# Performance work log

Measured on AMD Instinct MI355X. Metric: run time of the kernel, lower is better.

## Reference

```python
import jax, jax.numpy as jnp
import numpy as np

N = 100000
DEG = 16            # edges per source node (1 self-loop + 15 random)
E = N * DEG
IN_F = 128
OUT_F = 64
ALPHA = 0.2         # leaky relu negative slope


def _build_edges(key):
    # edges sorted by src (as adj.nonzero() would be), every node has >=1 out-edge
    src = jnp.repeat(jnp.arange(N, dtype=jnp.int32), DEG)
    dst = jax.random.randint(key, (E,), 0, N, dtype=jnp.int32)
    # force a self-loop as the first edge of every block
    self_pos = jnp.arange(E, dtype=jnp.int32) % DEG == 0
    dst = jnp.where(self_pos, src, dst)
    return jnp.stack([src, dst])  # [2, E]


def setup_inputs() -> dict:
    key = jax.random.key(0)
    k1, k2, k3, k4, k5, k6 = jax.random.split(key, 6)
    return {
        "input": jax.random.normal(k1, (N, IN_F), dtype=jnp.float32),
        "edge": _build_edges(k2),
        "W_high": jax.random.normal(k3, (IN_F, OUT_F), dtype=jnp.float32) * 0.1,
        "W_low": jax.random.normal(k4, (IN_F, OUT_F), dtype=jnp.float32) * 0.1,
        "a_high": jax.random.normal(k5, (1, 2 * OUT_F), dtype=jnp.float32) * 0.1,
        "a_low": jax.random.normal(k6, (1, 2 * OUT_F), dtype=jnp.float32) * 0.1,
    }


def _relu6(x):
    return jnp.clip(x, 0.0, 6.0)


def reference(input, edge, W_high, W_low, a_high, a_low):
    n = input.shape[0]
    src, dst = edge[0], edge[1]

    h_high = input @ W_high          # [N, F]
    h_low = input @ W_low            # [N, F]

    # a.mm(cat(h[src], h[dst]).T) == (h @ a_src)[src] + (h @ a_dst)[dst]
    f = W_high.shape[1]
    s_high = (h_high @ a_high[0, :f])[src] + (h_high @ a_high[0, f:])[dst]  # [E]
    s_low = (h_low @ a_low[0, :f])[src] + (h_low @ a_low[0, f:])[dst]

    edge_e_high = jnp.exp(-jax.nn.leaky_relu(s_high, ALPHA))  # [E], > 0
    edge_e_low = jnp.exp(-jax.nn.leaky_relu(s_low, ALPHA))

    seg = lambda v: jax.ops.segment_sum(v, src, num_segments=n, indices_are_sorted=True)

    # rowsum uses RAW exp values (before relu6/dropout), matching the source
    e_high_rowsum = seg(edge_e_high)[:, None]  # [N, 1]
    e_low_rowsum = seg(edge_e_low)[:, None]

    # relu6 clamp (dropout p=0 -> identity, eval mode)
    eh = _relu6(edge_e_high)
    el = _relu6(edge_e_low)

    # m @ (h[src] +/- h[dst]) == segment_sum over src of per-edge features
    h_agg_high = seg(h_high[src] + h_high[dst])   # [N, F]
    h_agg_low = seg(h_low[src] - h_low[dst])      # [N, F]

    # spmm: out[i] = sum_{(i,j)} e_ij * h_agg[j]
    h_prime_high = seg(eh[:, None] * h_agg_high[dst]) / e_high_rowsum
    h_prime_low = seg(el[:, None] * h_agg_low[dst]) / e_low_rowsum

    h_prime = 0.5 * (h_prime_high + h_prime_low)
    return _relu6(h_prime)  # concat=True
```

## Files before the change

kernel.cpp:

```cpp
#include <hip/hip_runtime.h>

#define N_NODES 100000
#define DEG 16
#define IN_F 128
#define OUT_F 64
#define E_EDGES (N_NODES * DEG)

typedef __bf16 bf16x8 __attribute__((ext_vector_type(8)));
typedef unsigned short u16x8 __attribute__((ext_vector_type(8)));
typedef float f32x4 __attribute__((ext_vector_type(4)));
typedef unsigned int u32x4 __attribute__((ext_vector_type(4)));

union BF8 { u16x8 u; bf16x8 b; };

__device__ inline float lo_bf(unsigned int u) {
    union { unsigned int i; float f; } v; v.i = u << 16; return v.f;
}
__device__ inline float hi_bf(unsigned int u) {
    union { unsigned int i; float f; } v; v.i = u & 0xFFFF0000u; return v.f;
}
__device__ inline unsigned short f2bf(float f) {
    union { float f; unsigned int i; } v; v.f = f;
    return (unsigned short)((v.i + 0x7FFFu + ((v.i >> 16) & 1u)) >> 16);
}
__device__ inline unsigned int packbf(float a, float b) {
    return (unsigned int)f2bf(a) | ((unsigned int)f2bf(b) << 16);
}

__global__ __launch_bounds__(256) void k_wprep(
    const float* __restrict__ Wh, const float* __restrict__ Wl,
    unsigned short* __restrict__ Wimg)
{
    int idx = blockIdx.x * 256 + threadIdx.x;
    int m = idx >> 13;
    int rem = idx & 8191;
    int k = rem >> 6, n = rem & 63;
    float v = m ? Wl[rem] : Wh[rem];
    Wimg[m * 8704 + n * 136 + k] = f2bf(v);
}

__global__ __launch_bounds__(256) void k_gemm(
    const float* __restrict__ in, const unsigned short* __restrict__ Wimg,
    unsigned int* __restrict__ H)
{
    __shared__ __align__(16) unsigned short ldsW[2][64][136];
    __shared__ __align__(16) unsigned short ldsA[64][136];

    {
        const u32x4* src = (const u32x4*)Wimg;
        u32x4* dst = (u32x4*)ldsW;
        for (int i = threadIdx.x; i < 2176; i += 256) dst[i] = src[i];
    }

    int row0B = blockIdx.x * 64;
    {
        const f32x4* src = (const f32x4*)(in + (size_t)row0B * IN_F);
        #pragma unroll
        for (int i = 0; i < 8; i++) {
            int c = threadIdx.x + 256 * i;
            int row = c >> 5;
            int kc = (c & 31) * 4;
            int grow = row0B + row;
            f32x4 v = (grow < N_NODES) ? src[c]
                      : *(const f32x4*)(in + (size_t)(N_NODES - 1) * IN_F + kc);
            unsigned int p0 = packbf(v[0], v[1]);
            unsigned int p1 = packbf(v[2], v[3]);
            *(unsigned int*)&ldsA[row][kc]     = p0;
            *(unsigned int*)&ldsA[row][kc + 2] = p1;
        }
    }
    __syncthreads();

    int wv = threadIdx.x >> 6;
    int lane = threadIdx.x & 63;
    int quad = lane >> 4, c = lane & 15;
    int row0 = row0B + wv * 16;

    bf16x8 afrag[4];
    #pragma unroll
    for (int kb = 0; kb < 4; kb++) {
        BF8 a;
        a.u = *(const u16x8*)&ldsA[wv * 16 + c][kb * 32 + quad * 8];
        afrag[kb] = a.b;
    }

    f32x4 acc[2][4];
    #pragma unroll
    for (int m = 0; m < 2; m++)
        #pragma unroll
        for (int t = 0; t < 4; t++) acc[m][t] = (f32x4){0, 0, 0, 0};

    #pragma unroll
    for (int kb = 0; kb < 4; kb++) {
        #pragma unroll
        for (int t = 0; t < 4; t++) {
            int n = t * 16 + c;
            BF8 bh, bl;
            bh.u = *(const u16x8*)&ldsW[0][n][kb * 32 + quad * 8];
            bl.u = *(const u16x8*)&ldsW[1][n][kb * 32 + quad * 8];
            acc[0][t] = __builtin_amdgcn_mfma_f32_16x16x32_bf16(afrag[kb], bh.b, acc[0][t], 0, 0, 0);
            acc[1][t] = __builtin_amdgcn_mfma_f32_16x16x32_bf16(afrag[kb], bl.b, acc[1][t], 0, 0, 0);
        }
    }

    #pragma unroll
    for (int r = 0; r < 4; r++) {
        int row = row0 + quad * 4 + r;
        if (row >= N_NODES) continue;
        size_t base = (size_t)row * OUT_F + c;
        #pragma unroll
        for (int t = 0; t < 4; t++)
            H[base + t * 16] = packbf(acc[0][t][r], acc[1][t][r]);
    }
}

__global__ __launch_bounds__(256) void k_agg(
    const unsigned int* __restrict__ H, const int* __restrict__ dst,
    const float* __restrict__ ah, const float* __restrict__ al,
    unsigned int* __restrict__ HAGG, f32x4* __restrict__ s)
{
    int lane = threadIdx.x & 63;
    int node = __builtin_amdgcn_readfirstlane(blockIdx.x * 4 + (threadIdx.x >> 6));
    const int* dp = dst + node * DEG;

    unsigned int hu = H[(size_t)node * 64 + lane];
    float hh = lo_bf(hu);
    float hl = hi_bf(hu);
    float sh = 16.0f * hh;
    float sl = 16.0f * hl;

    #pragma unroll
    for (int half = 0; half < 2; half++) {
        unsigned int u[8];
        #pragma unroll
        for (int t = 0; t < 8; t++) {
            int j = dp[half * 8 + t];
            u[t] = H[(size_t)j * 64 + lane];
        }
        #pragma unroll
        for (int t = 0; t < 8; t++) { sh += lo_bf(u[t]); sl -= hi_bf(u[t]); }
    }
    HAGG[(size_t)node * 64 + lane] = packbf(sh, sl);

    float ph = hh * ah[lane];
    float qh = hh * ah[64 + lane];
    float pl = hl * al[lane];
    float ql = hl * al[64 + lane];
    #pragma unroll
    for (int o = 32; o > 0; o >>= 1) {
        ph += __shfl_xor(ph, o);
        qh += __shfl_xor(qh, o);
        pl += __shfl_xor(pl, o);
        ql += __shfl_xor(ql, o);
    }
    if (lane == 0) s[node] = (f32x4){ph, qh, pl, ql};
}

__global__ __launch_bounds__(256) void k_out(
    const unsigned int* __restrict__ HAGG, const int* __restrict__ dst,
    const f32x4* __restrict__ s, float* __restrict__ out)
{
    int lane = threadIdx.x & 63;
    int node = __builtin_amdgcn_readfirstlane(blockIdx.x * 4 + (threadIdx.x >> 6));
    const int* dp = dst + node * DEG;

    int jl = dp[lane & 15];
    f32x4 si = s[node];
    f32x4 sj = s[jl];
    float xh = si.x + sj.y;
    float xl = si.z + sj.w;
    float lh = xh > 0.0f ? xh : 0.2f * xh;
    float ll = xl > 0.0f ? xl : 0.2f * xl;
    float wh = __expf(-lh);
    float wl = __expf(-ll);
    float rh = wh, rl = wl;
    #pragma unroll
    for (int o = 8; o > 0; o >>= 1) { rh += __shfl_xor(rh, o); rl += __shfl_xor(rl, o); }
    float eh = fminf(wh, 6.0f);
    float el = fminf(wl, 6.0f);

    float acc_h = 0.0f, acc_l = 0.0f;
    #pragma unroll
    for (int half = 0; half < 2; half++) {
        unsigned int u[8];
        float weh[8], wel[8];
        #pragma unroll
        for (int t = 0; t < 8; t++) {
            int j = dp[half * 8 + t];
            u[t] = HAGG[(size_t)j * 64 + lane];
        }
        #pragma unroll
        for (int t = 0; t < 8; t++) {
            weh[t] = __shfl(eh, half * 8 + t);
            wel[t] = __shfl(el, half * 8 + t);
        }
        #pragma unroll
        for (int t = 0; t < 8; t++) {
            acc_h += weh[t] * lo_bf(u[t]);
            acc_l += wel[t] * hi_bf(u[t]);
        }
    }
    float r = 0.5f * (acc_h / rh + acc_l / rl);
    r = fminf(fmaxf(r, 0.0f), 6.0f);
    out[(size_t)node * 64 + lane] = r;
}

extern "C" void kernel_launch(void* const* d_in, const int* in_sizes, int n_in,
                              void* d_out, int out_size, void* d_ws, size_t ws_size,
                              hipStream_t stream) {
    const float* input = (const float*)d_in[0];
    const int*   edge  = (const int*)d_in[1];
    const float* Wh    = (const float*)d_in[2];
    const float* Wl    = (const float*)d_in[3];
    const float* ah    = (const float*)d_in[4];
    const float* al    = (const float*)d_in[5];
    float* out = (float*)d_out;

    unsigned int* H    = (unsigned int*)d_ws;
    unsigned int* HAGG = H + (size_t)N_NODES * 64;
    f32x4* s = (f32x4*)(HAGG + (size_t)N_NODES * 64);
    unsigned short* Wimg = (unsigned short*)(s + N_NODES);

    const int* dstp = edge + E_EDGES;

    k_wprep<<<64, 256, 0, stream>>>(Wh, Wl, Wimg);
    k_gemm<<<1563, 256, 0, stream>>>(input, Wimg, H);
    k_agg<<<N_NODES / 4, 256, 0, stream>>>(H, dstp, ah, al, HAGG, s);
    k_out<<<N_NODES / 4, 256, 0, stream>>>(HAGG, dstp, s, out);
}
```

Before: 228.8 us.

## Store aggregated features in feature-group-major layout and split output gather by groups

HAGG is now written in 8 feature-group slabs (each slab holds 8 features per node, 32 bytes), and the output kernel is restructured so each block handles one feature group for 32 nodes, with 8 lanes per node. Keeping each pass over a single group slab shrinks the working set of the random neighbor gathers (1/8 of HAGG per group) so it can stay resident in cache across blocks. The trade-offs are that edge weights (exp/leaky-relu and s lookups) are recomputed 8 times per node, and each gather touches only 32 contiguous bytes per neighbor instead of 256.

```diff
diff --git a/kernel.cpp b/kernel.cpp
--- a/kernel.cpp
+++ b/kernel.cpp
@@ -117,7 +117,7 @@
 __global__ __launch_bounds__(256) void k_agg(
     const unsigned int* __restrict__ H, const int* __restrict__ dst,
     const float* __restrict__ ah, const float* __restrict__ al,
-    unsigned int* __restrict__ HAGG, f32x4* __restrict__ s)
+    unsigned int* __restrict__ HAGG_G, f32x4* __restrict__ s)
 {
     int lane = threadIdx.x & 63;
     int node = __builtin_amdgcn_readfirstlane(blockIdx.x * 4 + (threadIdx.x >> 6));
@@ -140,7 +140,7 @@
         #pragma unroll
         for (int t = 0; t < 8; t++) { sh += lo_bf(u[t]); sl -= hi_bf(u[t]); }
     }
-    HAGG[(size_t)node * 64 + lane] = packbf(sh, sl);
+    HAGG_G[((size_t)(lane >> 3) * N_NODES + node) * 8 + (lane & 7)] = packbf(sh, sl);
 
     float ph = hh * ah[lane];
     float qh = hh * ah[64 + lane];
@@ -156,53 +156,63 @@
     if (lane == 0) s[node] = (f32x4){ph, qh, pl, ql};
 }
 
-__global__ __launch_bounds__(256) void k_out(
-    const unsigned int* __restrict__ HAGG, const int* __restrict__ dst,
+__global__ __launch_bounds__(256) void k_out8(
+    const unsigned int* __restrict__ HAGG_G, const int* __restrict__ dst,
     const f32x4* __restrict__ s, float* __restrict__ out)
 {
     int lane = threadIdx.x & 63;
-    int node = __builtin_amdgcn_readfirstlane(blockIdx.x * 4 + (threadIdx.x >> 6));
-    const int* dp = dst + node * DEG;
-
-    int jl = dp[lane & 15];
+    int wv = threadIdx.x >> 6;
+    int g = blockIdx.x / 3125;
+    int b = blockIdx.x - g * 3125;
+    int n = lane >> 3, f = lane & 7;
+    int node = b * 32 + wv * 8 + n;
+
+    const unsigned int* base = HAGG_G + (size_t)g * N_NODES * 8 + f;
+
+    int2 jj = *(const int2*)&dst[node * DEG + f * 2];
     f32x4 si = s[node];
-    f32x4 sj = s[jl];
-    float xh = si.x + sj.y;
-    float xl = si.z + sj.w;
-    float lh = xh > 0.0f ? xh : 0.2f * xh;
-    float ll = xl > 0.0f ? xl : 0.2f * xl;
-    float wh = __expf(-lh);
-    float wl = __expf(-ll);
-    float rh = wh, rl = wl;
-    #pragma unroll
-    for (int o = 8; o > 0; o >>= 1) { rh += __shfl_xor(rh, o); rl += __shfl_xor(rl, o); }
-    float eh = fminf(wh, 6.0f);
-    float el = fminf(wl, 6.0f);
+    f32x4 sj0 = s[jj.x];
+    f32x4 sj1 = s[jj.y];
+    float xh0 = si.x + sj0.y, xl0 = si.z + sj0.w;
+    float xh1 = si.x + sj1.y, xl1 = si.z + sj1.w;
+    float lh0 = xh0 > 0.0f ? xh0 : 0.2f * xh0;
+    float ll0 = xl0 > 0.0f ? xl0 : 0.2f * xl0;
+    float lh1 = xh1 > 0.0f ? xh1 : 0.2f * xh1;
+    float ll1 = xl1 > 0.0f ? xl1 : 0.2f * xl1;
+    float wh0 = __expf(-lh0), wl0 = __expf(-ll0);
+    float wh1 = __expf(-lh1), wl1 = __expf(-ll1);
+
+    float rh = wh0 + wh1, rl = wl0 + wl1;
+    #pragma unroll
+    for (int o = 1; o < 8; o <<= 1) { rh += __shfl_xor(rh, o); rl += __shfl_xor(rl, o); }
+
+    float eh0 = fminf(wh0, 6.0f), el0 = fminf(wl0, 6.0f);
+    float eh1 = fminf(wh1, 6.0f), el1 = fminf(wl1, 6.0f);
+
+    int grpbase = lane & 0x38;
+    int jt[16]; float weh[16], wel[16];
+    #pragma unroll
+    for (int t = 0; t < 16; t++) {
+        int srcl = grpbase | (t >> 1);
+        jt[t]  = __shfl((t & 1) ? jj.y : jj.x, srcl);
+        weh[t] = __shfl((t & 1) ? eh1 : eh0, srcl);
+        wel[t] = __shfl((t & 1) ? el1 : el0, srcl);
+    }
+
+    unsigned int u[16];
+    #pragma unroll
+    for (int t = 0; t < 16; t++) u[t] = base[(size_t)jt[t] * 8];
 
     float acc_h = 0.0f, acc_l = 0.0f;
     #pragma unroll
-    for (int half = 0; half < 2; half++) {
-        unsigned int u[8];
-        float weh[8], wel[8];
-        #pragma unroll
-        for (int t = 0; t < 8; t++) {
-            int j = dp[half * 8 + t];
-            u[t] = HAGG[(size_t)j * 64 + lane];
-        }
-        #pragma unroll
-        for (int t = 0; t < 8; t++) {
-            weh[t] = __shfl(eh, half * 8 + t);
-            wel[t] = __shfl(el, half * 8 + t);
-        }
-        #pragma unroll
-        for (int t = 0; t < 8; t++) {
-            acc_h += weh[t] * lo_bf(u[t]);
-            acc_l += wel[t] * hi_bf(u[t]);
-        }
-    }
+    for (int t = 0; t < 16; t++) {
+        acc_h += weh[t] * lo_bf(u[t]);
+        acc_l += wel[t] * hi_bf(u[t]);
+    }
+
     float r = 0.5f * (acc_h / rh + acc_l / rl);
     r = fminf(fmaxf(r, 0.0f), 6.0f);
-    out[(size_t)node * 64 + lane] = r;
+    out[(size_t)node * 64 + g * 8 + f] = r;
 }
 
 extern "C" void kernel_launch(void* const* d_in, const int* in_sizes, int n_in,
@@ -216,15 +226,15 @@
     const float* al    = (const float*)d_in[5];
     float* out = (float*)d_out;
 
-    unsigned int* H    = (unsigned int*)d_ws;
-    unsigned int* HAGG = H + (size_t)N_NODES * 64;
-    f32x4* s = (f32x4*)(HAGG + (size_t)N_NODES * 64);
+    unsigned int* H      = (unsigned int*)d_ws;
+    unsigned int* HAGG_G = H + (size_t)N_NODES * 64;
+    f32x4* s = (f32x4*)(HAGG_G + (size_t)N_NODES * 64);
     unsigned short* Wimg = (unsigned short*)(s + N_NODES);
 
     const int* dstp = edge + E_EDGES;
 
     k_wprep<<<64, 256, 0, stream>>>(Wh, Wl, Wimg);
     k_gemm<<<1563, 256, 0, stream>>>(input, Wimg, H);
-    k_agg<<<N_NODES / 4, 256, 0, stream>>>(H, dstp, ah, al, HAGG, s);
-    k_out<<<N_NODES / 4, 256, 0, stream>>>(HAGG, dstp, s, out);
-}
+    k_agg<<<N_NODES / 4, 256, 0, stream>>>(H, dstp, ah, al, HAGG_G, s);
+    k_out8<<<25000, 256, 0, stream>>>(HAGG_G, dstp, s, out);
+}
```

After: 302.3 us. 32.1% more time.
